# Kernel optimization log

Hardware: AMD Instinct MI355X
Metric: run time of the kernel (lower is better)

Reference implementation:

```python
import jax, jax.numpy as jnp
import numpy as np

N = 50000      # nodes
E = 800000     # edges (avg degree 16)
D = 128        # in_dim = hidden_dim
C = 40         # num_classes
BN_EPS = 1e-5


def setup_inputs() -> dict:
    key = jax.random.key(0)
    ks = jax.random.split(key, 24)
    h = jax.random.normal(ks[0], (N, D), dtype=jnp.float32)
    edge_src = jax.random.randint(ks[1], (E,), 0, N)
    edge_dst = jax.random.randint(ks[2], (E,), 0, N)
    mask = jnp.ones((E, 1), dtype=jnp.float32)  # adj_mask2_fixed (frozen)

    def lin_w(k, fi, fo):
        return jax.random.normal(k, (fi, fo), dtype=jnp.float32) / np.sqrt(fi).astype(np.float32)

    def lin_b(k, fo):
        return jax.random.normal(k, (fo,), dtype=jnp.float32) * 0.01

    dims = [(D, D), (D, D), (D, C)]  # last GIN layer -> num_classes
    out = {"h": h, "edge_src": edge_src, "edge_dst": edge_dst, "mask": mask}
    for i, (fi, fo) in enumerate(dims):
        out[f"w{i}"] = lin_w(ks[3 + 4 * i], fi, fo)
        out[f"b{i}"] = lin_b(ks[4 + 4 * i], fo)
        out[f"g{i}"] = jnp.ones((fo,), jnp.float32) + 0.05 * jax.random.normal(ks[5 + 4 * i], (fo,), jnp.float32)
        out[f"beta{i}"] = 0.05 * jax.random.normal(ks[6 + 4 * i], (fo,), jnp.float32)
        out[f"rm{i}"] = 0.1 * jax.random.normal(jax.random.fold_in(key, 100 + i), (fo,), jnp.float32)
        out[f"rv{i}"] = jax.random.uniform(jax.random.fold_in(key, 200 + i), (fo,), jnp.float32, 0.5, 1.5)
    out["wp"] = lin_w(ks[20], D, C)
    out["bp"] = lin_b(ks[21], C)
    return out


def reference(h, edge_src, edge_dst, mask,
              w0, b0, g0, beta0, rm0, rv0,
              w1, b1, g1, beta1, rm1, rv1,
              w2, b2, g2, beta2, rm2, rv2,
              wp, bp):
    # in-degree for mean aggregation (DGL mean reducer: divide by in-degree,
    # zero for isolated nodes)
    ones_e = jnp.ones(edge_dst.shape, dtype=h.dtype)
    deg = jax.ops.segment_sum(ones_e, edge_dst, num_segments=N)
    deg_inv = jnp.where(deg > 0, 1.0 / jnp.maximum(deg, 1.0), 0.0)[:, None]

    def gin_layer(x, w, b, g, beta, rm, rv):
        msg = x[edge_src] * mask                                   # [E, d]
        agg = jax.ops.segment_sum(msg, edge_dst, num_segments=N) * deg_inv
        z = (x + agg) @ w + b                                      # (1+eps)=1, eps=0
        z = (z - rm) * jax.lax.rsqrt(rv + BN_EPS) * g + beta       # BN (eval, running stats)
        return jax.nn.relu(z)                                      # dropout: eval -> identity

    h1 = gin_layer(h, w0, b0, g0, beta0, rm0, rv0)    # [N, D]
    h2 = gin_layer(h1, w1, b1, g1, beta1, rm1, rv1)   # [N, D]  hidden_rep[-2]
    h3 = gin_layer(h2, w2, b2, g2, beta2, rm2, rv2)   # [N, C]  hidden_rep[-1]
    return ((h2 @ wp + bp) + h3) * 0.5
```

## Files before the change

kernel.cpp:

```cpp
#include <hip/hip_runtime.h>

#define N_NODES 50000
#define N_EDGES 800000
#define DIM 128
#define NCLS 40

#define NCHUNK 128
#define CE 6250
#define HALF_N 25088
#define WHALF 12544
#define SCAN_B 98
#define N_PAD 50432

typedef __bf16 bf16x8_t __attribute__((ext_vector_type(8)));
typedef unsigned short us8_t __attribute__((ext_vector_type(8)));
typedef float f32x4_t __attribute__((ext_vector_type(4)));

static __device__ __forceinline__ float b2f(unsigned short h) {
    unsigned u = ((unsigned)h) << 16;
    return __builtin_bit_cast(float, u);
}
static __device__ __forceinline__ unsigned short f2b(float f) {
    unsigned u = __builtin_bit_cast(unsigned, f);
    u += 0x7FFFu + ((u >> 16) & 1u);
    return (unsigned short)(u >> 16);
}

#define PREP_B 3125
#define REPACK_B 176
__global__ __launch_bounds__(256) void prep(const float* __restrict__ hsrc,
                                            unsigned short* __restrict__ hout,
                                            const float* __restrict__ w0,
                                            const float* __restrict__ w1,
                                            const float* __restrict__ w2,
                                            const float* __restrict__ wp,
                                            unsigned short* __restrict__ f0h,
                                            unsigned short* __restrict__ f0l,
                                            unsigned short* __restrict__ f1h,
                                            unsigned short* __restrict__ f1l,
                                            unsigned short* __restrict__ f2h,
                                            unsigned short* __restrict__ f2l,
                                            unsigned short* __restrict__ fph,
                                            unsigned short* __restrict__ fpl) {
    if (blockIdx.x < PREP_B) {
        size_t e0 = ((size_t)blockIdx.x * 256 + threadIdx.x) * 8;
        f32x4_t v0 = *(const f32x4_t*)(hsrc + e0);
        f32x4_t v1 = *(const f32x4_t*)(hsrc + e0 + 4);
        us8_t o;
        #pragma unroll
        for (int j = 0; j < 4; ++j) { o[j] = f2b(v0[j]); o[4 + j] = f2b(v1[j]); }
        *(us8_t*)(hout + e0) = o;
        return;
    }
    int t = (blockIdx.x - PREP_B) * 256 + threadIdx.x;
    const float* src;
    unsigned short *dh, *dl;
    int idx, ncols;
    if (t < 16384)      { src = w0; dh = f0h; dl = f0l; idx = t;         ncols = 128; }
    else if (t < 32768) { src = w1; dh = f1h; dl = f1l; idx = t - 16384; ncols = 128; }
    else if (t < 38912) { src = w2; dh = f2h; dl = f2l; idx = t - 32768; ncols = 48; }
    else if (t < 45056) { src = wp; dh = fph; dl = fpl; idx = t - 38912; ncols = 48; }
    else return;
    int k = idx / ncols, n = idx - k * ncols;
    float v;
    if (ncols == 128) v = src[k * 128 + n];
    else              v = (n < NCLS) ? src[k * NCLS + n] : 0.f;
    int nt = n >> 4, m = n & 15, kt = k >> 5, quad = (k >> 3) & 3, j = k & 7;
    int off = ((nt * 4 + kt) * 64 + quad * 16 + m) * 8 + j;
    unsigned short hi = f2b(v);
    dh[off] = hi;
    dl[off] = f2b(v - b2f(hi));
}

__global__ __launch_bounds__(256) void chunk_count(const int* __restrict__ dst,
                                                   unsigned* __restrict__ cnt) {
    __shared__ unsigned lds[WHALF];
    int c = blockIdx.x, h = blockIdx.y, tid = threadIdx.x;
    for (int w = tid; w < WHALF; w += 256) lds[w] = 0;
    __syncthreads();
    int base = c * CE;
    for (int k = tid; k < CE; k += 256) {
        int local = dst[base + k] - h * HALF_N;
        if (local >= 0 && local < HALF_N)
            atomicAdd(&lds[local >> 1], 1u << ((local & 1) * 16));
    }
    __syncthreads();
    unsigned* out = cnt + ((size_t)(h * NCHUNK + c)) * WHALF;
    for (int w = tid; w < WHALF; w += 256) out[w] = lds[w];
}

__global__ __launch_bounds__(256) void cscan(unsigned* __restrict__ cnt,
                                             unsigned* __restrict__ degp,
                                             int* __restrict__ partial) {
    __shared__ int lds[256];
    int b = blockIdx.x;
    int h = b / 49;
    int w = (b % 49) * 256 + threadIdx.x;
    unsigned acc = 0;
    for (int c = 0; c < NCHUNK; ++c) {
        size_t idx = ((size_t)(h * NCHUNK + c)) * WHALF + w;
        unsigned v = cnt[idx];
        cnt[idx] = acc;
        acc += v;
    }
    degp[h * WHALF + w] = acc;
    lds[threadIdx.x] = (int)(acc & 0xFFFFu) + (int)(acc >> 16);
    __syncthreads();
    #pragma unroll
    for (int off = 128; off > 0; off >>= 1) {
        if (threadIdx.x < off) lds[threadIdx.x] += lds[threadIdx.x + off];
        __syncthreads();
    }
    if (threadIdx.x == 0) partial[b] = lds[0];
}

__global__ __launch_bounds__(256) void scan_final(const unsigned* __restrict__ degp,
                                                  const int* __restrict__ partial,
                                                  int* __restrict__ rs,
                                                  int* __restrict__ deg,
                                                  float* __restrict__ dinv) {
    __shared__ int lds[256];
    int b = blockIdx.x;
    int h = b / 49;
    int tid = threadIdx.x;
    int w = (b % 49) * 256 + tid;
    lds[tid] = (tid < b) ? partial[tid] : 0;
    __syncthreads();
    #pragma unroll
    for (int off = 128; off > 0; off >>= 1) {
        if (tid < off) lds[tid] += lds[tid + off];
        __syncthreads();
    }
    int boff = lds[0];
    __syncthreads();
    unsigned dp = degp[h * WHALF + w];
    int lo = (int)(dp & 0xFFFFu), hi = (int)(dp >> 16);
    int s = lo + hi;
    lds[tid] = s;
    __syncthreads();
    #pragma unroll
    for (int off = 1; off < 256; off <<= 1) {
        int v = lds[tid];
        int add = (tid >= off) ? lds[tid - off] : 0;
        __syncthreads();
        lds[tid] = v + add;
        __syncthreads();
    }
    int excl = boff + lds[tid] - s;
    int n0 = h * HALF_N + 2 * w;
    rs[n0] = excl;
    rs[n0 + 1] = excl + lo;
    deg[n0] = lo;
    deg[n0 + 1] = hi;
    dinv[n0] = (lo > 0) ? (1.0f / (float)lo) : 0.0f;
    dinv[n0 + 1] = (hi > 0) ? (1.0f / (float)hi) : 0.0f;
}

__global__ __launch_bounds__(256) void fill2(const int* __restrict__ src,
                                             const int* __restrict__ dst,
                                             const float* __restrict__ mask,
                                             const unsigned* __restrict__ cnt,
                                             const int* __restrict__ rs,
                                             unsigned* __restrict__ csr) {
    __shared__ unsigned cur[WHALF];
    int c = blockIdx.x, h = blockIdx.y, tid = threadIdx.x;
    const unsigned* off = cnt + ((size_t)(h * NCHUNK + c)) * WHALF;
    for (int w = tid; w < WHALF; w += 256) cur[w] = off[w];
    __syncthreads();
    int base = c * CE;
    for (int k = tid; k < CE; k += 256) {
        int e = base + k;
        int d = dst[e];
        int local = d - h * HALF_N;
        if (local >= 0 && local < HALF_N) {
            unsigned sm = (unsigned)src[e] | ((unsigned)f2b(mask[e]) << 16);
            int sh = (local & 1) * 16;
            unsigned old = atomicAdd(&cur[local >> 1], 1u << sh);
            int rank = (int)((old >> sh) & 0xFFFFu);
            csr[rs[d] + rank] = sm;
        }
    }
}

static __device__ __forceinline__ void issue16(const unsigned short* __restrict__ xb,
                                               unsigned pk, int lane, unsigned* vv) {
    #pragma unroll
    for (int j = 0; j < 16; ++j) {
        unsigned p = (unsigned)__builtin_amdgcn_readlane((int)pk, j);
        vv[j] = *(const unsigned*)(xb + (size_t)(p & 0xFFFFu) * DIM + lane * 2);
    }
}
static __device__ __forceinline__ void accum16(unsigned pk, const unsigned* vv,
                                               float& acc0, float& acc1) {
    #pragma unroll
    for (int j = 0; j < 16; ++j) {
        unsigned p = (unsigned)__builtin_amdgcn_readlane((int)pk, j);
        float mm = b2f((unsigned short)(p >> 16));
        acc0 += mm * b2f((unsigned short)(vv[j] & 0xFFFFu));
        acc1 += mm * b2f((unsigned short)(vv[j] >> 16));
    }
}

template<bool RES32>
static __device__ __forceinline__ void gather4(const unsigned short* __restrict__ xb,
                                               const float* __restrict__ xres,
                                               const unsigned short* __restrict__ xlo,
                                               const int* __restrict__ rs,
                                               const int* __restrict__ deg,
                                               const float* __restrict__ dinv,
                                               const unsigned* __restrict__ csr,
                                               int nb0, int lane,
                                               float (*ldsrow)[132], int row0) {
    int rs4[4], dg4[4];
    float di4[4];
    #pragma unroll
    for (int i = 0; i < 4; ++i) {
        int n = nb0 + i;
        rs4[i] = rs[n];
        dg4[i] = deg[n];
        di4[i] = dinv[n];
    }
    unsigned pk0, pk1, pk2, pk3;
    pk0 = (lane < (dg4[0] < 16 ? dg4[0] : 16)) ? csr[rs4[0] + lane] : 0u;
    pk1 = (lane < (dg4[1] < 16 ? dg4[1] : 16)) ? csr[rs4[1] + lane] : 0u;

    unsigned vvA[16], vvB[16];
    issue16(xb, pk0, lane, vvA);

    unsigned pkq[4] = {pk0, pk1, 0u, 0u};
    #pragma unroll
    for (int i = 0; i < 4; ++i) {
        if (i == 0) pk2 = (lane < (dg4[2] < 16 ? dg4[2] : 16)) ? csr[rs4[2] + lane] : 0u;
        if (i == 1) pk3 = (lane < (dg4[3] < 16 ? dg4[3] : 16)) ? csr[rs4[3] + lane] : 0u;
        if (i == 0) pkq[2] = pk2;
        if (i == 1) pkq[3] = pk3;
        if (i < 3) issue16(xb, pkq[i + 1], lane, (i & 1) ? vvA : vvB);
        float acc0 = 0.f, acc1 = 0.f;
        accum16(pkq[i], (i & 1) ? vvB : vvA, acc0, acc1);
        for (int base = 16; base < dg4[i]; base += 16) {
            int nb = dg4[i] - base;
            if (nb > 16) nb = 16;
            unsigned pke = (lane < nb) ? csr[rs4[i] + base + lane] : 0u;
            unsigned vvE[16];
            issue16(xb, pke, lane, vvE);
            accum16(pke, vvE, acc0, acc1);
        }
        float di = di4[i];
        float x0, x1;
        if constexpr (RES32) {
            float2 xp = *(const float2*)(xres + (size_t)(nb0 + i) * DIM + lane * 2);
            x0 = xp.x; x1 = xp.y;
        } else {
            unsigned hv = *(const unsigned*)(xb  + (size_t)(nb0 + i) * DIM + lane * 2);
            unsigned lv = *(const unsigned*)(xlo + (size_t)(nb0 + i) * DIM + lane * 2);
            x0 = b2f((unsigned short)(hv & 0xFFFFu)) + b2f((unsigned short)(lv & 0xFFFFu));
            x1 = b2f((unsigned short)(hv >> 16))     + b2f((unsigned short)(lv >> 16));
        }
        ldsrow[row0 + i][lane * 2]     = x0 + acc0 * di;
        ldsrow[row0 + i][lane * 2 + 1] = x1 + acc1 * di;
    }
}

template<bool RES32>
__global__ __launch_bounds__(256) void fused_layer(const unsigned short* __restrict__ xb,
                                                   const float* __restrict__ xres,
                                                   const unsigned short* __restrict__ xlo,
                                                   const int* __restrict__ rs,
                                                   const int* __restrict__ deg,
                                                   const float* __restrict__ dinv,
                                                   const unsigned* __restrict__ csr,
                                                   const unsigned short* __restrict__ wfh,
                                                   const unsigned short* __restrict__ wfl,
                                                   const float* __restrict__ bias,
                                                   const float* __restrict__ gam,
                                                   const float* __restrict__ bet,
                                                   const float* __restrict__ rm,
                                                   const float* __restrict__ rv,
                                                   unsigned short* __restrict__ outhi,
                                                   unsigned short* __restrict__ outlo) {
    __shared__ float lds[16][132];
    int tid = threadIdx.x;
    int wave = tid >> 6, lane = tid & 63;
    int rbase = blockIdx.x * 16;

    gather4<RES32>(xb, xres, xlo, rs, deg, dinv, csr, rbase + wave * 4, lane, lds, wave * 4);
    __syncthreads();

    int m = lane & 15, quad = lane >> 4;
    const float* ap = &lds[m][0];

    us8_t ah[4], al[4];
    #pragma unroll
    for (int kt = 0; kt < 4; ++kt) {
        f32x4_t p0 = *(const f32x4_t*)(ap + kt * 32 + quad * 8);
        f32x4_t p1 = *(const f32x4_t*)(ap + kt * 32 + quad * 8 + 4);
        #pragma unroll
        for (int j = 0; j < 4; ++j) {
            unsigned short h0 = f2b(p0[j]);
            unsigned short h1 = f2b(p1[j]);
            ah[kt][j] = h0;
            ah[kt][4 + j] = h1;
            al[kt][j] = f2b(p0[j] - b2f(h0));
            al[kt][4 + j] = f2b(p1[j] - b2f(h1));
        }
    }

    f32x4_t acc[2] = {};
    #pragma unroll
    for (int kt = 0; kt < 4; ++kt) {
        #pragma unroll
        for (int t = 0; t < 2; ++t) {
            int nt = wave * 2 + t;
            int boff = ((nt * 4 + kt) * 64 + lane) * 8;
            us8_t bh = *(const us8_t*)(wfh + boff);
            us8_t bl = *(const us8_t*)(wfl + boff);
            acc[t] = __builtin_amdgcn_mfma_f32_16x16x32_bf16(
                __builtin_bit_cast(bf16x8_t, ah[kt]),
                __builtin_bit_cast(bf16x8_t, bh), acc[t], 0, 0, 0);
            acc[t] = __builtin_amdgcn_mfma_f32_16x16x32_bf16(
                __builtin_bit_cast(bf16x8_t, ah[kt]),
                __builtin_bit_cast(bf16x8_t, bl), acc[t], 0, 0, 0);
            acc[t] = __builtin_amdgcn_mfma_f32_16x16x32_bf16(
                __builtin_bit_cast(bf16x8_t, al[kt]),
                __builtin_bit_cast(bf16x8_t, bh), acc[t], 0, 0, 0);
        }
    }

    #pragma unroll
    for (int t = 0; t < 2; ++t) {
        int nt = wave * 2 + t;
        int j = nt * 16 + m;
        float bj = bias[j];
        float sc = gam[j] * rsqrtf(rv[j] + 1e-5f);
        float sh = bet[j] - rm[j] * sc;
        #pragma unroll
        for (int i = 0; i < 4; ++i) {
            int r = rbase + quad * 4 + i;
            float z = fmaxf((acc[t][i] + bj) * sc + sh, 0.f);
            unsigned short zh = f2b(z);
            outhi[(size_t)r * DIM + j] = zh;
            outlo[(size_t)r * DIM + j] = f2b(z - b2f(zh));
        }
    }
}

__global__ __launch_bounds__(256) void fused_final2(const unsigned short* __restrict__ xb,
                                                    const unsigned short* __restrict__ xlo,
                                                    const int* __restrict__ rs,
                                                    const int* __restrict__ deg,
                                                    const float* __restrict__ dinv,
                                                    const unsigned* __restrict__ csr,
                                                    const unsigned short* __restrict__ f2h,
                                                    const unsigned short* __restrict__ f2l,
                                                    const unsigned short* __restrict__ fph,
                                                    const unsigned short* __restrict__ fpl,
                                                    const float* __restrict__ b2,
                                                    const float* __restrict__ g2,
                                                    const float* __restrict__ be2,
                                                    const float* __restrict__ rm2,
                                                    const float* __restrict__ rv2,
                                                    const float* __restrict__ bp,
                                                    float* __restrict__ out) {
    __shared__ float lds[16][132];
    int tid = threadIdx.x;
    int wave = tid >> 6, lane = tid & 63;
    int rbase = blockIdx.x * 16;

    gather4<false>(xb, nullptr, xlo, rs, deg, dinv, csr, rbase + wave * 4, lane, lds, wave * 4);
    __syncthreads();

    if (wave == 3) return;

    int m = lane & 15, quad = lane >> 4;
    int arow = rbase + m;
    const float* ap2 = &lds[m][0];
    const unsigned short* aphh = xb  + (size_t)arow * DIM;
    const unsigned short* aphl = xlo + (size_t)arow * DIM;

    us8_t a2h[4], a2l[4], ahh[4], ahl[4];
    #pragma unroll
    for (int kt = 0; kt < 4; ++kt) {
        f32x4_t p0 = *(const f32x4_t*)(ap2 + kt * 32 + quad * 8);
        f32x4_t p1 = *(const f32x4_t*)(ap2 + kt * 32 + quad * 8 + 4);
        ahh[kt] = *(const us8_t*)(aphh + kt * 32 + quad * 8);
        ahl[kt] = *(const us8_t*)(aphl + kt * 32 + quad * 8);
        #pragma unroll
        for (int j = 0; j < 4; ++j) {
            unsigned short h0 = f2b(p0[j]), h1 = f2b(p1[j]);
            a2h[kt][j] = h0; a2h[kt][4 + j] = h1;
            a2l[kt][j] = f2b(p0[j] - b2f(h0));
            a2l[kt][4 + j] = f2b(p1[j] - b2f(h1));
        }
    }

    int nt = wave;
    f32x4_t acc2 = {};
    f32x4_t accp = {};
    #pragma unroll
    for (int kt = 0; kt < 4; ++kt) {
        int boff = ((nt * 4 + kt) * 64 + lane) * 8;
        us8_t b2hv = *(const us8_t*)(f2h + boff);
        us8_t b2lv = *(const us8_t*)(f2l + boff);
        us8_t bphv = *(const us8_t*)(fph + boff);
        us8_t bplv = *(const us8_t*)(fpl + boff);
        acc2 = __builtin_amdgcn_mfma_f32_16x16x32_bf16(
            __builtin_bit_cast(bf16x8_t, a2h[kt]),
            __builtin_bit_cast(bf16x8_t, b2hv), acc2, 0, 0, 0);
        acc2 = __builtin_amdgcn_mfma_f32_16x16x32_bf16(
            __builtin_bit_cast(bf16x8_t, a2h[kt]),
            __builtin_bit_cast(bf16x8_t, b2lv), acc2, 0, 0, 0);
        acc2 = __builtin_amdgcn_mfma_f32_16x16x32_bf16(
            __builtin_bit_cast(bf16x8_t, a2l[kt]),
            __builtin_bit_cast(bf16x8_t, b2hv), acc2, 0, 0, 0);
        accp = __builtin_amdgcn_mfma_f32_16x16x32_bf16(
            __builtin_bit_cast(bf16x8_t, ahh[kt]),
            __builtin_bit_cast(bf16x8_t, bphv), accp, 0, 0, 0);
        accp = __builtin_amdgcn_mfma_f32_16x16x32_bf16(
            __builtin_bit_cast(bf16x8_t, ahh[kt]),
            __builtin_bit_cast(bf16x8_t, bplv), accp, 0, 0, 0);
        accp = __builtin_amdgcn_mfma_f32_16x16x32_bf16(
            __builtin_bit_cast(bf16x8_t, ahl[kt]),
            __builtin_bit_cast(bf16x8_t, bphv), accp, 0, 0, 0);
    }

    int j = nt * 16 + m;
    if (j < NCLS) {
        float b2j = b2[j];
        float sc = g2[j] * rsqrtf(rv2[j] + 1e-5f);
        float sh = be2[j] - rm2[j] * sc;
        float bpj = bp[j];
        #pragma unroll
        for (int i = 0; i < 4; ++i) {
            int r = rbase + quad * 4 + i;
            float z = fmaxf((acc2[i] + b2j) * sc + sh, 0.f);
            float p = accp[i] + bpj;
            out[(size_t)r * NCLS + j] = (p + z) * 0.5f;
        }
    }
}

extern "C" void kernel_launch(void* const* d_in, const int* in_sizes, int n_in,
                              void* d_out, int out_size, void* d_ws, size_t ws_size,
                              hipStream_t stream) {
    const float* h    = (const float*)d_in[0];
    const int* esrc   = (const int*)d_in[1];
    const int* edst   = (const int*)d_in[2];
    const float* mask = (const float*)d_in[3];
    const float* w0   = (const float*)d_in[4];
    const float* b0   = (const float*)d_in[5];
    const float* g0   = (const float*)d_in[6];
    const float* be0  = (const float*)d_in[7];
    const float* rm0  = (const float*)d_in[8];
    const float* rv0  = (const float*)d_in[9];
    const float* w1   = (const float*)d_in[10];
    const float* b1   = (const float*)d_in[11];
    const float* g1   = (const float*)d_in[12];
    const float* be1  = (const float*)d_in[13];
    const float* rm1  = (const float*)d_in[14];
    const float* rv1  = (const float*)d_in[15];
    const float* w2   = (const float*)d_in[16];
    const float* b2   = (const float*)d_in[17];
    const float* g2   = (const float*)d_in[18];
    const float* be2  = (const float*)d_in[19];
    const float* rm2  = (const float*)d_in[20];
    const float* rv2  = (const float*)d_in[21];
    const float* wp   = (const float*)d_in[22];
    const float* bp   = (const float*)d_in[23];

    char* ws = (char*)d_ws;
    size_t off = 0;
    auto alloc = [&](size_t bytes) {
        char* p = ws + off;
        off = (off + bytes + 255) & ~(size_t)255;
        return p;
    };
    int* rs       = (int*)alloc(N_PAD * 4);
    int* deg      = (int*)alloc(N_PAD * 4);
    float* dinv   = (float*)alloc(N_PAD * 4);
    int* partial  = (int*)alloc(128 * 4);
    unsigned* degp = (unsigned*)alloc(2 * WHALF * 4);
    unsigned* csr = (unsigned*)alloc((size_t)N_EDGES * 4);
    unsigned* cnt = (unsigned*)alloc((size_t)2 * NCHUNK * WHALF * 4);
    unsigned short* xb16   = (unsigned short*)alloc((size_t)N_NODES * DIM * 2);
    unsigned short* hbA_hi = (unsigned short*)alloc((size_t)N_NODES * DIM * 2);
    unsigned short* hbA_lo = (unsigned short*)alloc((size_t)N_NODES * DIM * 2);
    unsigned short* hbB_hi = (unsigned short*)alloc((size_t)N_NODES * DIM * 2);
    unsigned short* hbB_lo = (unsigned short*)alloc((size_t)N_NODES * DIM * 2);
    unsigned short* f0h = (unsigned short*)alloc(16384 * 2);
    unsigned short* f0l = (unsigned short*)alloc(16384 * 2);
    unsigned short* f1h = (unsigned short*)alloc(16384 * 2);
    unsigned short* f1l = (unsigned short*)alloc(16384 * 2);
    unsigned short* f2h = (unsigned short*)alloc(6144 * 2);
    unsigned short* f2l = (unsigned short*)alloc(6144 * 2);
    unsigned short* fph = (unsigned short*)alloc(6144 * 2);
    unsigned short* fpl = (unsigned short*)alloc(6144 * 2);

    const int GB16 = N_NODES / 16;

    prep<<<PREP_B + REPACK_B, 256, 0, stream>>>(h, xb16, w0, w1, w2, wp,
                                                f0h, f0l, f1h, f1l, f2h, f2l, fph, fpl);
    chunk_count<<<dim3(NCHUNK, 2), 256, 0, stream>>>(edst, cnt);
    cscan<<<SCAN_B, 256, 0, stream>>>(cnt, degp, partial);
    scan_final<<<SCAN_B, 256, 0, stream>>>(degp, partial, rs, deg, dinv);
    fill2<<<dim3(NCHUNK, 2), 256, 0, stream>>>(esrc, edst, mask, cnt, rs, csr);

    fused_layer<true><<<GB16, 256, 0, stream>>>(xb16, h, xb16, rs, deg, dinv, csr,
                                                f0h, f0l, b0, g0, be0, rm0, rv0,
                                                hbA_hi, hbA_lo);
    fused_layer<false><<<GB16, 256, 0, stream>>>(hbA_hi, h, hbA_lo, rs, deg, dinv, csr,
                                                 f1h, f1l, b1, g1, be1, rm1, rv1,
                                                 hbB_hi, hbB_lo);
    fused_final2<<<GB16, 256, 0, stream>>>(hbB_hi, hbB_lo, rs, deg, dinv, csr,
                                           f2h, f2l, fph, fpl,
                                           b2, g2, be2, rm2, rv2, bp, (float*)d_out);
}
```

Baseline: 296.5 us.

## Split column scan over chunks into four segments for more parallelism

The per-word scan over 128 chunks is split into 4 segments of 32 chunks, so the launch has 392 blocks instead of 98, each walking a shorter serial loop. Per-segment totals are combined in scan_final into segment offsets, which fill2 adds back when seeding its LDS cursors. Block partial sums are accumulated with atomics into a buffer zeroed by chunk_count. The cost is extra segsum/segoff traffic and one more load per word in fill2.

New measurement: 286.1 us. 3.5% less time.

```diff
diff --git a/kernel.cpp b/kernel.cpp
--- a/kernel.cpp
+++ b/kernel.cpp
@@ -10,6 +10,8 @@
 #define HALF_N 25088
 #define WHALF 12544
 #define SCAN_B 98
+#define NSEG 4
+#define SEGC 32
 #define N_PAD 50432
 
 typedef __bf16 bf16x8_t __attribute__((ext_vector_type(8)));
@@ -73,9 +75,11 @@
 }
 
 __global__ __launch_bounds__(256) void chunk_count(const int* __restrict__ dst,
-                                                   unsigned* __restrict__ cnt) {
+                                                   unsigned* __restrict__ cnt,
+                                                   int* __restrict__ partial) {
     __shared__ unsigned lds[WHALF];
     int c = blockIdx.x, h = blockIdx.y, tid = threadIdx.x;
+    if (c == 0 && h == 0 && tid < 128) partial[tid] = 0;
     for (int w = tid; w < WHALF; w += 256) lds[w] = 0;
     __syncthreads();
     int base = c * CE;
@@ -89,21 +93,24 @@
     for (int w = tid; w < WHALF; w += 256) out[w] = lds[w];
 }
 
-__global__ __launch_bounds__(256) void cscan(unsigned* __restrict__ cnt,
-                                             unsigned* __restrict__ degp,
-                                             int* __restrict__ partial) {
-    __shared__ int lds[256];
-    int b = blockIdx.x;
+__global__ __launch_bounds__(256) void cscan_seg(unsigned* __restrict__ cnt,
+                                                 unsigned* __restrict__ segsum,
+                                                 int* __restrict__ partial) {
+    int bx = blockIdx.x;
+    int seg = bx / SCAN_B;
+    int b = bx - seg * SCAN_B;
     int h = b / 49;
     int w = (b % 49) * 256 + threadIdx.x;
     unsigned acc = 0;
-    for (int c = 0; c < NCHUNK; ++c) {
+    int c0 = seg * SEGC;
+    for (int c = c0; c < c0 + SEGC; ++c) {
         size_t idx = ((size_t)(h * NCHUNK + c)) * WHALF + w;
         unsigned v = cnt[idx];
         cnt[idx] = acc;
         acc += v;
     }
-    degp[h * WHALF + w] = acc;
+    segsum[((size_t)(seg * 2 + h)) * WHALF + w] = acc;
+    __shared__ int lds[256];
     lds[threadIdx.x] = (int)(acc & 0xFFFFu) + (int)(acc >> 16);
     __syncthreads();
     #pragma unroll
@@ -111,10 +118,11 @@
         if (threadIdx.x < off) lds[threadIdx.x] += lds[threadIdx.x + off];
         __syncthreads();
     }
-    if (threadIdx.x == 0) partial[b] = lds[0];
-}
-
-__global__ __launch_bounds__(256) void scan_final(const unsigned* __restrict__ degp,
+    if (threadIdx.x == 0) atomicAdd(&partial[b], lds[0]);
+}
+
+__global__ __launch_bounds__(256) void scan_final(const unsigned* __restrict__ segsum,
+                                                  unsigned* __restrict__ segoff,
                                                   const int* __restrict__ partial,
                                                   int* __restrict__ rs,
                                                   int* __restrict__ deg,
@@ -124,7 +132,7 @@
     int h = b / 49;
     int tid = threadIdx.x;
     int w = (b % 49) * 256 + tid;
-    lds[tid] = (tid < b) ? partial[tid] : 0;
+    lds[tid] = (tid < b && tid < 128) ? partial[tid] : 0;
     __syncthreads();
     #pragma unroll
     for (int off = 128; off > 0; off >>= 1) {
@@ -133,7 +141,16 @@
     }
     int boff = lds[0];
     __syncthreads();
-    unsigned dp = degp[h * WHALF + w];
+    size_t wb = (size_t)h * WHALF + w;
+    unsigned run = 0;
+    unsigned dp = 0;
+    #pragma unroll
+    for (int s = 0; s < NSEG; ++s) {
+        unsigned sv = segsum[((size_t)(s * 2 + h)) * WHALF + w];
+        segoff[((size_t)(s * 2 + h)) * WHALF + w] = run;
+        run += sv;
+    }
+    dp = run;
     int lo = (int)(dp & 0xFFFFu), hi = (int)(dp >> 16);
     int s = lo + hi;
     lds[tid] = s;
@@ -147,7 +164,8 @@
         __syncthreads();
     }
     int excl = boff + lds[tid] - s;
-    int n0 = h * HALF_N + 2 * w;
+    int n0 = h * HALF_N + 2 * ((b % 49) * 256 + tid);
+    (void)wb;
     rs[n0] = excl;
     rs[n0 + 1] = excl + lo;
     deg[n0] = lo;
@@ -160,12 +178,15 @@
                                              const int* __restrict__ dst,
                                              const float* __restrict__ mask,
                                              const unsigned* __restrict__ cnt,
+                                             const unsigned* __restrict__ segoff,
                                              const int* __restrict__ rs,
                                              unsigned* __restrict__ csr) {
     __shared__ unsigned cur[WHALF];
     int c = blockIdx.x, h = blockIdx.y, tid = threadIdx.x;
+    int seg = c >> 5;
     const unsigned* off = cnt + ((size_t)(h * NCHUNK + c)) * WHALF;
-    for (int w = tid; w < WHALF; w += 256) cur[w] = off[w];
+    const unsigned* soff = segoff + ((size_t)(seg * 2 + h)) * WHALF;
+    for (int w = tid; w < WHALF; w += 256) cur[w] = off[w] + soff[w];
     __syncthreads();
     int base = c * CE;
     for (int k = tid; k < CE; k += 256) {
@@ -478,7 +499,8 @@
     int* deg      = (int*)alloc(N_PAD * 4);
     float* dinv   = (float*)alloc(N_PAD * 4);
     int* partial  = (int*)alloc(128 * 4);
-    unsigned* degp = (unsigned*)alloc(2 * WHALF * 4);
+    unsigned* segsum = (unsigned*)alloc((size_t)NSEG * 2 * WHALF * 4);
+    unsigned* segoff = (unsigned*)alloc((size_t)NSEG * 2 * WHALF * 4);
     unsigned* csr = (unsigned*)alloc((size_t)N_EDGES * 4);
     unsigned* cnt = (unsigned*)alloc((size_t)2 * NCHUNK * WHALF * 4);
     unsigned short* xb16   = (unsigned short*)alloc((size_t)N_NODES * DIM * 2);
@@ -499,10 +521,10 @@
 
     prep<<<PREP_B + REPACK_B, 256, 0, stream>>>(h, xb16, w0, w1, w2, wp,
                                                 f0h, f0l, f1h, f1l, f2h, f2l, fph, fpl);
-    chunk_count<<<dim3(NCHUNK, 2), 256, 0, stream>>>(edst, cnt);
-    cscan<<<SCAN_B, 256, 0, stream>>>(cnt, degp, partial);
-    scan_final<<<SCAN_B, 256, 0, stream>>>(degp, partial, rs, deg, dinv);
-    fill2<<<dim3(NCHUNK, 2), 256, 0, stream>>>(esrc, edst, mask, cnt, rs, csr);
+    chunk_count<<<dim3(NCHUNK, 2), 256, 0, stream>>>(edst, cnt, partial);
+    cscan_seg<<<SCAN_B * NSEG, 256, 0, stream>>>(cnt, segsum, partial);
+    scan_final<<<SCAN_B, 256, 0, stream>>>(segsum, segoff, partial, rs, deg, dinv);
+    fill2<<<dim3(NCHUNK, 2), 256, 0, stream>>>(esrc, edst, mask, cnt, segoff, rs, csr);
 
     fused_layer<true><<<GB16, 256, 0, stream>>>(xb16, h, xb16, rs, deg, dinv, csr,
                                                 f0h, f0l, b0, g0, be0, rm0, rv0,
```
